# Performance work log

Measured on AMD Instinct MI355X. Metric: run time of the kernel, lower is better.

The kernel has to match this reference:

```python
import jax, jax.numpy as jnp
import numpy as np

Z_DIM = 3
H = 128
N_BLOCKS = 4
N = 30000
E = 180000
T = 2


def _mlp2(x, W1, b1, W2, b2):
    return jnp.maximum(x @ W1 + b1, 0.0) @ W2 + b2


def _stats(x, eps=1e-8):
    # batch mean/std as accumulated by the running-stat Normalizer (buffers -> no grad)
    m = x.mean(0)
    v = jnp.maximum((x * x).mean(0) - m * m, 0.0)
    s = jnp.maximum(jnp.sqrt(v), eps)
    return jax.lax.stop_gradient(m), jax.lax.stop_gradient(s)


def setup_inputs() -> dict:
    key = jax.random.key(0)
    ks = jax.random.split(key, 32)

    def w(k, shape, fan_in):
        return jax.random.normal(k, shape, jnp.float32) / np.sqrt(fan_in).astype(np.float32)

    inp = {}
    inp["z"] = jax.random.normal(ks[0], (T, N, Z_DIM), jnp.float32)
    inp["z_target"] = jax.random.normal(ks[1], (N, Z_DIM), jnp.float32)
    inp["pos"] = jax.random.uniform(ks[2], (N, 2), jnp.float32)
    # encoder node MLP: z_dim -> H -> H
    inp["enc_node_W1"] = w(ks[3], (Z_DIM, H), Z_DIM)
    inp["enc_node_b1"] = jnp.zeros((H,), jnp.float32)
    inp["enc_node_W2"] = w(ks[4], (H, H), H)
    inp["enc_node_b2"] = jnp.zeros((H,), jnp.float32)
    # encoder edge MLP: edge_dim(3) -> H -> H
    inp["enc_edge_W1"] = w(ks[5], (3, H), 3)
    inp["enc_edge_b1"] = jnp.zeros((H,), jnp.float32)
    inp["enc_edge_W2"] = w(ks[6], (H, H), H)
    inp["enc_edge_b2"] = jnp.zeros((H,), jnp.float32)
    # decoder MLP: H -> H -> z_dim
    inp["dec_W1"] = w(ks[7], (H, H), H)
    inp["dec_b1"] = jnp.zeros((H,), jnp.float32)
    inp["dec_W2"] = w(ks[8], (H, Z_DIM), H)
    inp["dec_b2"] = jnp.zeros((Z_DIM,), jnp.float32)
    # GraphNetBlocks, stacked over n_blocks
    inp["blk_edge_W1"] = w(ks[9], (N_BLOCKS, 3 * H, H), 3 * H)
    inp["blk_edge_b1"] = jnp.zeros((N_BLOCKS, H), jnp.float32)
    inp["blk_edge_W2"] = w(ks[10], (N_BLOCKS, H, H), H)
    inp["blk_edge_b2"] = jnp.zeros((N_BLOCKS, H), jnp.float32)
    inp["blk_node_W1"] = w(ks[11], (N_BLOCKS, 2 * H, H), 2 * H)
    inp["blk_node_b1"] = jnp.zeros((N_BLOCKS, H), jnp.float32)
    inp["blk_node_W2"] = w(ks[12], (N_BLOCKS, H, H), H)
    inp["blk_node_b2"] = jnp.zeros((N_BLOCKS, H), jnp.float32)
    # bidirectional mesh edges (triangles_to_edges output)
    inp["senders"] = jax.random.randint(ks[13], (E,), 0, N, jnp.int64)
    inp["receivers"] = jax.random.randint(ks[14], (E,), 0, N, jnp.int64)
    return inp


def reference(z, z_target, pos,
              enc_node_W1, enc_node_b1, enc_node_W2, enc_node_b2,
              enc_edge_W1, enc_edge_b1, enc_edge_W2, enc_edge_b2,
              dec_W1, dec_b1, dec_W2, dec_b2,
              blk_edge_W1, blk_edge_b1, blk_edge_W2, blk_edge_b2,
              blk_node_W1, blk_node_b1, blk_node_W2, blk_node_b2,
              senders, receivers):
    zl = z[-1]                                   # [N, z_dim]
    n_nodes = zl.shape[0]

    # --- build_graph ---
    rel = pos[senders] - pos[receivers]          # [E, 2]
    ef_raw = jnp.concatenate([rel, jnp.linalg.norm(rel, axis=1, keepdims=True)], axis=1)  # [E, 3]
    em, es = _stats(ef_raw)
    ef = _mlp2((ef_raw - em) / es, enc_edge_W1, enc_edge_b1, enc_edge_W2, enc_edge_b2)    # [E, H]
    nm, ns = _stats(zl)
    nf = _mlp2((zl - nm) / ns, enc_node_W1, enc_node_b1, enc_node_W2, enc_node_b2)        # [N, H]

    # --- message passing blocks ---
    def block(carry, p):
        nf, ef = carry
        eW1, eb1, eW2, eb2, nW1, nb1, nW2, nb2 = p
        e_in = jnp.concatenate([ef, nf[senders], nf[receivers]], axis=1)   # [E, 3H]
        ef = _mlp2(e_in, eW1, eb1, eW2, eb2) + ef
        agg = jax.ops.segment_sum(ef, receivers, num_segments=n_nodes)    # [N, H]
        n_in = jnp.concatenate([nf, agg], axis=1)                          # [N, 2H]
        nf = _mlp2(n_in, nW1, nb1, nW2, nb2) + nf
        return (nf, ef), None

    (nf, ef), _ = jax.lax.scan(block, (nf, ef),
                               (blk_edge_W1, blk_edge_b1, blk_edge_W2, blk_edge_b2,
                                blk_node_W1, blk_node_b1, blk_node_W2, blk_node_b2))

    # --- decode + loss ---
    output = _mlp2(nf, dec_W1, dec_b1, dec_W2, dec_b2)                     # [N, z_dim]
    target = z_target - zl
    om, os = _stats(target)
    target_normalized = (target - om) / os
    loss = jnp.mean((target_normalized - output) ** 2)

    z_update = jax.lax.stop_gradient(output) * os + om                     # Normalizer.inverse(detach)
    z_pred = zl + z_update
    rmse = jnp.mean(jnp.sqrt(jnp.mean((z_pred - z_target) ** 2, axis=0)))
    return z_pred, loss, rmse
```

## Files before the change

### kernel.cpp

```cpp
#include <hip/hip_runtime.h>
#include <hip/hip_bf16.h>
#include <math.h>

#define HDIM 128
#define TPB 256

typedef __attribute__((ext_vector_type(8))) short bf16x8;
typedef __attribute__((ext_vector_type(4))) float f32x4;

static inline int ceil_div(int a, int b){ return (a + b - 1) / b; }

__device__ __forceinline__ float wave_sum(float v){
#pragma unroll
  for (int o = 32; o > 0; o >>= 1) v += __shfl_down(v, o, 64);
  return v;
}

__device__ __forceinline__ short f2bf(float f){
  __hip_bfloat16 h = __float2bfloat16(f);
  return *reinterpret_cast<short*>(&h);
}
__device__ __forceinline__ float bfb2f(short s){
  unsigned int u = ((unsigned int)(unsigned short)s) << 16;
  return __builtin_bit_cast(float, u);
}

__device__ __forceinline__ void gl_lds16(const short* g, short* l){
  __builtin_amdgcn_global_load_lds(
      (const __attribute__((address_space(1))) void*)g,
      (__attribute__((address_space(3))) void*)l, 16, 0, 0);
}

__global__ void csr_hist(const int* __restrict__ rcv, int* __restrict__ deg, int E){
  int e = blockIdx.x * blockDim.x + threadIdx.x;
  if (e < E) atomicAdd(&deg[rcv[e]], 1);
}

__global__ void csr_scan(const int* __restrict__ deg, int* __restrict__ row_start,
                         int N, int E){
  __shared__ int part[1024];
  int t = threadIdx.x;
  int chunk = (N + 1023) / 1024;
  int lo = t * chunk, hi = min(lo + chunk, N);
  int s = 0;
  for (int i = lo; i < hi; i++) s += deg[i];
  part[t] = s;
  __syncthreads();
  for (int off = 1; off < 1024; off <<= 1){
    int v = (t >= off) ? part[t - off] : 0;
    __syncthreads();
    part[t] += v;
    __syncthreads();
  }
  int base = (t == 0) ? 0 : part[t - 1];
  for (int i = lo; i < hi; i++){
    row_start[i] = base;
    base += deg[i];
  }
  if (t == 1023) row_start[N] = E;
}

__global__ void csr_scatter(const int* __restrict__ snd,
                            const int* __restrict__ rcv,
                            int* __restrict__ cursor,
                            int* __restrict__ pinv,
                            int* __restrict__ psnd,
                            int* __restrict__ prcv, int E){
  int e = blockIdx.x * blockDim.x + threadIdx.x;
  if (e < E){
    int r = rcv[e];
    int p = atomicAdd(&cursor[r], 1);
    pinv[e] = p;
    psnd[p] = snd[e];
    prcv[p] = r;
  }
}

__global__ void edge_raw_stats(const float* __restrict__ pos,
                               const int* __restrict__ snd,
                               const int* __restrict__ rcv,
                               const int* __restrict__ pinv,
                               float* __restrict__ ef_raw,
                               float* __restrict__ epart, int E){
  __shared__ float red[4][6];
  int tid = threadIdx.x, w = tid >> 6, l = tid & 63;
  int e = blockIdx.x * blockDim.x + tid;
  float s[6] = {0.f,0.f,0.f,0.f,0.f,0.f};
  if (e < E){
    int si = snd[e], ri = rcv[e];
    float rx = pos[2*si]   - pos[2*ri];
    float ry = pos[2*si+1] - pos[2*ri+1];
    float nm = sqrtf(rx*rx + ry*ry);
    int p = pinv[e];
    ef_raw[3*p]   = rx;
    ef_raw[3*p+1] = ry;
    ef_raw[3*p+2] = nm;
    s[0] = rx; s[1] = ry; s[2] = nm;
    s[3] = rx*rx; s[4] = ry*ry; s[5] = nm*nm;
  }
#pragma unroll
  for (int k = 0; k < 6; k++) s[k] = wave_sum(s[k]);
  if (l == 0)
#pragma unroll
    for (int k = 0; k < 6; k++) red[w][k] = s[k];
  __syncthreads();
  if (tid < 6)
    epart[(size_t)blockIdx.x * 6 + tid] =
      red[0][tid] + red[1][tid] + red[2][tid] + red[3][tid];
}

__global__ void node_stats(const float* __restrict__ zl,
                           const float* __restrict__ z_target,
                           float* __restrict__ npart, int N){
  __shared__ float red[4][12];
  int tid = threadIdx.x, w = tid >> 6, l = tid & 63;
  int n = blockIdx.x * blockDim.x + tid;
  float s[12];
#pragma unroll
  for (int i = 0; i < 12; i++) s[i] = 0.f;
  if (n < N){
#pragma unroll
    for (int d = 0; d < 3; d++){
      float z = zl[3*n+d];
      float t = z_target[3*n+d] - z;
      s[d]   = z;  s[3+d] = z*z;
      s[6+d] = t;  s[9+d] = t*t;
    }
  }
#pragma unroll
  for (int i = 0; i < 12; i++) s[i] = wave_sum(s[i]);
  if (l == 0)
#pragma unroll
    for (int i = 0; i < 12; i++) red[w][i] = s[i];
  __syncthreads();
  if (tid < 12)
    npart[(size_t)blockIdx.x * 12 + tid] =
      red[0][tid] + red[1][tid] + red[2][tid] + red[3][tid];
}

__global__ void reduce_stats(const float* __restrict__ ep, int ne,
                             const float* __restrict__ np_, int nn,
                             float* __restrict__ raw){
  __shared__ float red[4];
  int tid = threadIdx.x, w = tid >> 6, l = tid & 63;
  for (int j = 0; j < 6; j++){
    float s = 0.f;
    for (int b = tid; b < ne; b += 256) s += ep[(size_t)b * 6 + j];
    s = wave_sum(s);
    if (l == 0) red[w] = s;
    __syncthreads();
    if (tid == 0) raw[j] = red[0] + red[1] + red[2] + red[3];
    __syncthreads();
  }
  for (int j = 0; j < 12; j++){
    float s = 0.f;
    for (int b = tid; b < nn; b += 256) s += np_[(size_t)b * 12 + j];
    s = wave_sum(s);
    if (l == 0) red[w] = s;
    __syncthreads();
    if (tid == 0) raw[6 + j] = red[0] + red[1] + red[2] + red[3];
    __syncthreads();
  }
}

__global__ void finalize_stats(const float* __restrict__ raw,
                               float* __restrict__ fin, int E, int N){
#pragma unroll
  for (int d = 0; d < 3; d++){
    float cE = (float)E, cN = (float)N;
    float m, v;
    m = raw[0+d] / cE; v = fmaxf(raw[3+d]/cE - m*m, 0.f);
    fin[0+d] = m;  fin[3+d]  = fmaxf(sqrtf(v), 1e-8f);
    m = raw[6+d] / cN; v = fmaxf(raw[9+d]/cN - m*m, 0.f);
    fin[6+d] = m;  fin[9+d]  = fmaxf(sqrtf(v), 1e-8f);
    m = raw[12+d] / cN; v = fmaxf(raw[15+d]/cN - m*m, 0.f);
    fin[12+d] = m; fin[15+d] = fmaxf(sqrtf(v), 1e-8f);
  }
}

__global__ void pack_weights(const float* __restrict__ encEW2,
                             const float* __restrict__ encNW2,
                             const float* __restrict__ decW1,
                             const float* __restrict__ beW1,
                             const float* __restrict__ beW2,
                             const float* __restrict__ bnW1,
                             const float* __restrict__ bnW2,
                             __hip_bfloat16* __restrict__ wp){
  int y = blockIdx.y;
  const float* src; __hip_bfloat16* dst; int K;
  if (y == 0){ src = encEW2; dst = wp;          K = 128; }
  else if (y == 1){ src = encNW2; dst = wp + 16384; K = 128; }
  else if (y == 2){ src = decW1;  dst = wp + 32768; K = 128; }
  else {
    int b = (y - 3) >> 2, j = (y - 3) & 3;
    __hip_bfloat16* base = wp + 49152 + b * 114688;
    if (j == 0){ src = beW1 + b*49152; dst = base;          K = 384; }
    else if (j == 1){ src = beW2 + b*16384; dst = base + 49152; K = 128; }
    else if (j == 2){ src = bnW1 + b*32768; dst = base + 65536; K = 256; }
    else { src = bnW2 + b*16384; dst = base + 98304; K = 128; }
  }
  int id = blockIdx.x * blockDim.x + threadIdx.x;
  if (id >= 128 * K) return;
  int c = id >> 12;
  int r = id & 4095;
  int t = r >> 9;
  int l = (r >> 3) & 63;
  int j = r & 7;
  int k = c * 32 + ((l >> 4) << 3) + j;
  int n = t * 16 + (l & 15);
  dst[id] = __float2bfloat16(src[k * 128 + n]);
}

__launch_bounds__(256)
__global__ void encoder_fused(const float* __restrict__ raw,
                              const float* __restrict__ mptr,
                              const float* __restrict__ sptr,
                              const float* __restrict__ W1,
                              const float* __restrict__ b1,
                              const __hip_bfloat16* __restrict__ W2f,
                              const float* __restrict__ b2,
                              __hip_bfloat16* __restrict__ out, int rows){
  __shared__ __align__(16) short bsh[16384];
  const int tid = threadIdx.x, w = tid >> 6, l = tid & 63, m = l & 15, q = l >> 4;
  const short* wsrc = (const short*)W2f;
#pragma unroll
  for (int i = 0; i < 8; i++){
    int inst = w * 8 + i;
    gl_lds16(wsrc + inst * 512 + l * 8, &bsh[inst * 512]);
  }
  float s0 = mptr[0], s1 = mptr[1], s2 = mptr[2];
  float d0 = sptr[0], d1 = sptr[1], d2 = sptr[2];
  const int row0 = blockIdx.x * 64 + w * 16;
  const int ra = min(row0 + m, rows - 1);
  float x0 = (raw[3*ra]   - s0) / d0;
  float x1 = (raw[3*ra+1] - s1) / d1;
  float x2 = (raw[3*ra+2] - s2) / d2;
  bf16x8 afr[4];
#pragma unroll
  for (int c = 0; c < 4; c++){
    int nb = c * 32 + q * 8;
#pragma unroll
    for (int j = 0; j < 8; j++){
      float h = b1[nb+j] + x0 * W1[nb+j] + x1 * W1[128+nb+j] + x2 * W1[256+nb+j];
      afr[c][j] = f2bf(fmaxf(h, 0.f));
    }
  }
  f32x4 acc[8];
#pragma unroll
  for (int t = 0; t < 8; t++) acc[t] = (f32x4){0.f,0.f,0.f,0.f};
  __syncthreads();
#pragma unroll
  for (int c = 0; c < 4; c++){
#pragma unroll
    for (int t = 0; t < 8; t++){
      bf16x8 b = *(const bf16x8*)&bsh[(c*8 + t)*512 + l*8];
      acc[t] = __builtin_amdgcn_mfma_f32_16x16x32_bf16(afr[c], b, acc[t], 0, 0, 0);
    }
  }
  const int row_d = row0 + q * 4;
#pragma unroll
  for (int t = 0; t < 8; t++){
    int col = t * 16 + m;
    float bb = b2[col];
#pragma unroll
    for (int r = 0; r < 4; r++){
      int e = row_d + r;
      if (e < rows) out[(size_t)e * HDIM + col] = __float2bfloat16(acc[t][r] + bb);
    }
  }
}

__launch_bounds__(256)
__global__ void gemm128_g(const __hip_bfloat16* __restrict__ A,
                          const __hip_bfloat16* __restrict__ Wf,
                          const float* __restrict__ bias,
                          float* __restrict__ out, int rows){
  __shared__ __align__(16) short bsh[16384];
  const int tid = threadIdx.x, w = tid >> 6, l = tid & 63, m = l & 15, q = l >> 4;
  const short* wsrc = (const short*)Wf;
#pragma unroll
  for (int i = 0; i < 8; i++){
    int inst = w * 8 + i;
    gl_lds16(wsrc + inst * 512 + l * 8, &bsh[inst * 512]);
  }
  const int row0 = blockIdx.x * 64 + w * 16;
  const int ra = min(row0 + m, rows - 1);
  const short* pa = (const short*)A + (size_t)ra * HDIM + q * 8;
  bf16x8 afr[4];
#pragma unroll
  for (int c = 0; c < 4; c++) afr[c] = *(const bf16x8*)(pa + c * 32);
  f32x4 acc[8];
#pragma unroll
  for (int t = 0; t < 8; t++) acc[t] = (f32x4){0.f,0.f,0.f,0.f};
  __syncthreads();
#pragma unroll
  for (int c = 0; c < 4; c++){
#pragma unroll
    for (int t = 0; t < 8; t++){
      bf16x8 b = *(const bf16x8*)&bsh[(c*8 + t)*512 + l*8];
      acc[t] = __builtin_amdgcn_mfma_f32_16x16x32_bf16(afr[c], b, acc[t], 0, 0, 0);
    }
  }
  const int row_d = row0 + q * 4;
#pragma unroll
  for (int t = 0; t < 8; t++){
    int col = t * 16 + m;
    float bb = bias[col];
#pragma unroll
    for (int r = 0; r < 4; r++){
      int e = row_d + r;
      if (e < rows) out[(size_t)e * HDIM + col] = fmaxf(acc[t][r] + bb, 0.f);
    }
  }
}

__launch_bounds__(512)
__global__ void edge_block(const int* __restrict__ psnd,
                           const int* __restrict__ prcv,
                           const __hip_bfloat16* __restrict__ nf,
                           __hip_bfloat16* __restrict__ ef,
                           const __hip_bfloat16* __restrict__ Wfrag,
                           const float* __restrict__ b1,
                           const float* __restrict__ b2,
                           int E){
  __shared__ __align__(16) short bsh[2][4096];
  __shared__ __align__(16) short hsh[8][16][136];
  const int tid = threadIdx.x, w = tid >> 6, l = tid & 63, m = l & 15, q = l >> 4;
  const short* wsrc = (const short*)Wfrag;
  gl_lds16(wsrc + w*512 + l*8, &bsh[0][w*512]);

  const int row0 = blockIdx.x * 128 + w * 16;
  const int ra = min(row0 + m, E - 1);
  const int si = psnd[ra], ri = prcv[ra];
  const short* pe = (const short*)ef + (size_t)ra * HDIM + q * 8;
  const short* ps = (const short*)nf + (size_t)si * HDIM + q * 8;
  const short* pr = (const short*)nf + (size_t)ri * HDIM + q * 8;
  bf16x8 afr[12];
#pragma unroll
  for (int c = 0; c < 4; c++){
    afr[c]   = *(const bf16x8*)(pe + c * 32);
    afr[4+c] = *(const bf16x8*)(ps + c * 32);
    afr[8+c] = *(const bf16x8*)(pr + c * 32);
  }
  f32x4 acc[8];
#pragma unroll
  for (int t = 0; t < 8; t++) acc[t] = (f32x4){0.f,0.f,0.f,0.f};
  __syncthreads();
#pragma unroll
  for (int c = 0; c < 12; c++){
    gl_lds16(wsrc + (c+1)*4096 + w*512 + l*8, &bsh[(c+1)&1][w*512]);
    const short* bb = &bsh[c & 1][0];
#pragma unroll
    for (int t = 0; t < 8; t++){
      bf16x8 b = *(const bf16x8*)(bb + t*512 + l*8);
      acc[t] = __builtin_amdgcn_mfma_f32_16x16x32_bf16(afr[c], b, acc[t], 0, 0, 0);
    }
    __syncthreads();
  }
#pragma unroll
  for (int t = 0; t < 8; t++){
    float bb = b1[t * 16 + m];
#pragma unroll
    for (int r = 0; r < 4; r++)
      hsh[w][q*4 + r][t*16 + m] = f2bf(fmaxf(acc[t][r] + bb, 0.f));
  }
  const short* ph = &hsh[w][m][0] + q * 8;
  f32x4 acc2[8];
#pragma unroll
  for (int t = 0; t < 8; t++) acc2[t] = (f32x4){0.f,0.f,0.f,0.f};
#pragma unroll
  for (int c = 12; c < 16; c++){
    if (c + 1 < 16)
      gl_lds16(wsrc + (c+1)*4096 + w*512 + l*8, &bsh[(c+1)&1][w*512]);
    bf16x8 a = *(const bf16x8*)(ph + (c - 12) * 32);
    const short* bb = &bsh[c & 1][0];
#pragma unroll
    for (int t = 0; t < 8; t++){
      bf16x8 b = *(const bf16x8*)(bb + t*512 + l*8);
      acc2[t] = __builtin_amdgcn_mfma_f32_16x16x32_bf16(a, b, acc2[t], 0, 0, 0);
    }
    if (c < 15) __syncthreads();
  }
#pragma unroll
  for (int t = 0; t < 8; t++){
    float bb = b2[t * 16 + m];
#pragma unroll
    for (int r = 0; r < 4; r++)
      hsh[w][q*4 + r][t*16 + m] = f2bf(acc2[t][r] + bb);
  }
  int orow = row0 + (l >> 2);
  if (orow < E){
    const short* src = &hsh[w][l >> 2][(l & 3) * 32];
    short* dst = (short*)ef + (size_t)orow * HDIM + (l & 3) * 32;
#pragma unroll
    for (int k = 0; k < 4; k++){
      bf16x8 vnew = *(const bf16x8*)(src + k * 8);
      bf16x8 vold = *(const bf16x8*)(dst + k * 8);
      bf16x8 vo;
#pragma unroll
      for (int j = 0; j < 8; j++) vo[j] = f2bf(bfb2f(vnew[j]) + bfb2f(vold[j]));
      *(bf16x8*)(dst + k * 8) = vo;
    }
  }
}

__launch_bounds__(512)
__global__ void node_block(const int* __restrict__ row_start,
                           const __hip_bfloat16* __restrict__ ef,
                           __hip_bfloat16* __restrict__ nf,
                           const __hip_bfloat16* __restrict__ Wfrag,
                           const float* __restrict__ b1,
                           const float* __restrict__ b2,
                           int N){
  __shared__ __align__(16) short bsh[2][4096];
  __shared__ __align__(16) short hsh[8][16][136];
  const int tid = threadIdx.x, w = tid >> 6, l = tid & 63, m = l & 15, q = l >> 4;
  const short* wsrc = (const short*)Wfrag;
  gl_lds16(wsrc + w*512 + l*8, &bsh[0][w*512]);

  const int row0 = blockIdx.x * 128 + w * 16;
  const int ra = min(row0 + m, N - 1);
  const short* pn = (const short*)nf + (size_t)ra * HDIM + q * 8;
  bf16x8 afr[8];
#pragma unroll
  for (int c = 0; c < 4; c++) afr[c] = *(const bf16x8*)(pn + c * 32);
  float sum[4][8];
#pragma unroll
  for (int c = 0; c < 4; c++)
#pragma unroll
    for (int j = 0; j < 8; j++) sum[c][j] = 0.f;
  int s0 = row_start[ra], s1 = row_start[ra + 1];
  for (int it = s0; it < s1; it++){
    const short* pf = (const short*)ef + (size_t)it * HDIM + q * 8;
#pragma unroll
    for (int c = 0; c < 4; c++){
      bf16x8 v = *(const bf16x8*)(pf + c * 32);
#pragma unroll
      for (int j = 0; j < 8; j++) sum[c][j] += bfb2f(v[j]);
    }
  }
#pragma unroll
  for (int c = 0; c < 4; c++)
#pragma unroll
    for (int j = 0; j < 8; j++) afr[4 + c][j] = f2bf(sum[c][j]);

  f32x4 acc[8];
#pragma unroll
  for (int t = 0; t < 8; t++) acc[t] = (f32x4){0.f,0.f,0.f,0.f};
  __syncthreads();
#pragma unroll
  for (int c = 0; c < 8; c++){
    gl_lds16(wsrc + (c+1)*4096 + w*512 + l*8, &bsh[(c+1)&1][w*512]);
    const short* bb = &bsh[c & 1][0];
#pragma unroll
    for (int t = 0; t < 8; t++){
      bf16x8 b = *(const bf16x8*)(bb + t*512 + l*8);
      acc[t] = __builtin_amdgcn_mfma_f32_16x16x32_bf16(afr[c], b, acc[t], 0, 0, 0);
    }
    __syncthreads();
  }
#pragma unroll
  for (int t = 0; t < 8; t++){
    float bb = b1[t * 16 + m];
#pragma unroll
    for (int r = 0; r < 4; r++)
      hsh[w][q*4 + r][t*16 + m] = f2bf(fmaxf(acc[t][r] + bb, 0.f));
  }
  const short* ph = &hsh[w][m][0] + q * 8;
  f32x4 acc2[8];
#pragma unroll
  for (int t = 0; t < 8; t++) acc2[t] = (f32x4){0.f,0.f,0.f,0.f};
#pragma unroll
  for (int c = 8; c < 12; c++){
    if (c + 1 < 12)
      gl_lds16(wsrc + (c+1)*4096 + w*512 + l*8, &bsh[(c+1)&1][w*512]);
    bf16x8 a = *(const bf16x8*)(ph + (c - 8) * 32);
    const short* bb = &bsh[c & 1][0];
#pragma unroll
    for (int t = 0; t < 8; t++){
      bf16x8 b = *(const bf16x8*)(bb + t*512 + l*8);
      acc2[t] = __builtin_amdgcn_mfma_f32_16x16x32_bf16(a, b, acc2[t], 0, 0, 0);
    }
    if (c < 11) __syncthreads();
  }
#pragma unroll
  for (int t = 0; t < 8; t++){
    float bb = b2[t * 16 + m];
#pragma unroll
    for (int r = 0; r < 4; r++)
      hsh[w][q*4 + r][t*16 + m] = f2bf(acc2[t][r] + bb);
  }
  int orow = row0 + (l >> 2);
  if (orow < N){
    const short* src = &hsh[w][l >> 2][(l & 3) * 32];
    short* dst = (short*)nf + (size_t)orow * HDIM + (l & 3) * 32;
#pragma unroll
    for (int k = 0; k < 4; k++){
      bf16x8 vnew = *(const bf16x8*)(src + k * 8);
      bf16x8 vold = *(const bf16x8*)(dst + k * 8);
      bf16x8 vo;
#pragma unroll
      for (int j = 0; j < 8; j++) vo[j] = f2bf(bfb2f(vnew[j]) + bfb2f(vold[j]));
      *(bf16x8*)(dst + k * 8) = vo;
    }
  }
}

__global__ void dec_final(const float* __restrict__ hbuf,
                          const float* __restrict__ W2,
                          const float* __restrict__ b2,
                          float* __restrict__ outd, int rows){
  __shared__ float hl[64 * 129];
  __shared__ float Wl[HDIM * 3];
  __shared__ float bl[3];
  int t = threadIdx.x;
  int node0 = blockIdx.x * 64;
  for (int i = t; i < HDIM * 3; i += 256) Wl[i] = W2[i];
  if (t < 3) bl[t] = b2[t];
#pragma unroll
  for (int i = 0; i < 32; i++){
    int lin = t + i * 256;
    int r = lin >> 7;
    int c = lin & 127;
    int node = node0 + r;
    hl[r * 129 + c] = (node < rows) ? hbuf[(size_t)node * HDIM + c] : 0.f;
  }
  __syncthreads();
  if (t < 64){
    int node = node0 + t;
    if (node < rows){
      float a0 = bl[0], a1 = bl[1], a2 = bl[2];
      for (int k = 0; k < HDIM; k++){
        float v = hl[t * 129 + k];
        a0 += v * Wl[k * 3];
        a1 += v * Wl[k * 3 + 1];
        a2 += v * Wl[k * 3 + 2];
      }
      outd[3 * node]     = a0;
      outd[3 * node + 1] = a1;
      outd[3 * node + 2] = a2;
    }
  }
}

__global__ void epilogue(const float* __restrict__ dec_out,
                         const float* __restrict__ zl,
                         const float* __restrict__ z_target,
                         const float* __restrict__ fin,
                         float* __restrict__ d_out,
                         float* __restrict__ lpart, int N){
  __shared__ float red[4][4];
  int tid = threadIdx.x, w = tid >> 6, l = tid & 63;
  int n = blockIdx.x * blockDim.x + tid;
  float s[4] = {0.f,0.f,0.f,0.f};
  if (n < N){
#pragma unroll
    for (int d = 0; d < 3; d++){
      float om = fin[12 + d], os = fin[15 + d];
      float o   = dec_out[3*n + d];
      float zld = zl[3*n + d];
      float zt  = z_target[3*n + d];
      float tgt = zt - zld;
      float tn  = (tgt - om) / os;
      float diff = tn - o;
      s[0] += diff * diff;
      float zp = zld + o * os + om;
      d_out[3*n + d] = zp;
      float e = zp - zt;
      s[1 + d] = e * e;
    }
  }
#pragma unroll
  for (int k = 0; k < 4; k++) s[k] = wave_sum(s[k]);
  if (l == 0)
#pragma unroll
    for (int k = 0; k < 4; k++) red[w][k] = s[k];
  __syncthreads();
  if (tid < 4)
    lpart[(size_t)blockIdx.x * 4 + tid] =
      red[0][tid] + red[1][tid] + red[2][tid] + red[3][tid];
}

__global__ void finalize_out(const float* __restrict__ lpart, int nb,
                             float* __restrict__ d_out, int N){
  __shared__ float red[4];
  __shared__ float vals[4];
  int tid = threadIdx.x, w = tid >> 6, l = tid & 63;
  for (int j = 0; j < 4; j++){
    float s = 0.f;
    for (int b = tid; b < nb; b += 256) s += lpart[(size_t)b * 4 + j];
    s = wave_sum(s);
    if (l == 0) red[w] = s;
    __syncthreads();
    if (tid == 0) vals[j] = red[0] + red[1] + red[2] + red[3];
    __syncthreads();
  }
  if (tid == 0){
    float cN = (float)N;
    float loss = vals[0] / (3.f * cN);
    float rmse = (sqrtf(vals[1] / cN) + sqrtf(vals[2] / cN) + sqrtf(vals[3] / cN)) / 3.f;
    d_out[(size_t)3 * N]     = loss;
    d_out[(size_t)3 * N + 1] = rmse;
  }
}

extern "C" void kernel_launch(void* const* d_in, const int* in_sizes, int n_in,
                              void* d_out, int out_size, void* d_ws, size_t ws_size,
                              hipStream_t stream){
  const float* z           = (const float*)d_in[0];
  const float* z_target    = (const float*)d_in[1];
  const float* pos         = (const float*)d_in[2];
  const float* enc_node_W1 = (const float*)d_in[3];
  const float* enc_node_b1 = (const float*)d_in[4];
  const float* enc_node_W2 = (const float*)d_in[5];
  const float* enc_node_b2 = (const float*)d_in[6];
  const float* enc_edge_W1 = (const float*)d_in[7];
  const float* enc_edge_b1 = (const float*)d_in[8];
  const float* enc_edge_W2 = (const float*)d_in[9];
  const float* enc_edge_b2 = (const float*)d_in[10];
  const float* dec_W1      = (const float*)d_in[11];
  const float* dec_b1      = (const float*)d_in[12];
  const float* dec_W2      = (const float*)d_in[13];
  const float* dec_b2      = (const float*)d_in[14];
  const float* blk_edge_W1 = (const float*)d_in[15];
  const float* blk_edge_b1 = (const float*)d_in[16];
  const float* blk_edge_W2 = (const float*)d_in[17];
  const float* blk_edge_b2 = (const float*)d_in[18];
  const float* blk_node_W1 = (const float*)d_in[19];
  const float* blk_node_b1 = (const float*)d_in[20];
  const float* blk_node_W2 = (const float*)d_in[21];
  const float* blk_node_b2 = (const float*)d_in[22];
  const int*   senders     = (const int*)d_in[23];
  const int*   receivers   = (const int*)d_in[24];

  const int N = in_sizes[1] / 3;
  const int E = in_sizes[23];
  const float* zl = z + (size_t)N * 3;

  const int neb = ceil_div(E, TPB);
  const int nnb = ceil_div(N, TPB);

  char* p = (char*)d_ws;
  auto carve = [&](size_t bytes) -> char* {
    char* r = p; p += (bytes + 255) & ~(size_t)255; return r;
  };
  float* stats_raw = (float*)carve(32 * 4);
  float* stats_fin = (float*)carve(32 * 4);
  float* epart     = (float*)carve((size_t)neb * 6 * 4);
  float* npart     = (float*)carve((size_t)nnb * 12 * 4);
  float* lpart     = (float*)carve((size_t)nnb * 4 * 4);
  float* ef_raw    = (float*)carve((size_t)E * 3 * 4);
  float* dec_out   = (float*)carve((size_t)N * 3 * 4);
  float* hbuf      = (float*)carve((size_t)N * HDIM * 4);
  int*   deg       = (int*)carve((size_t)N * 4);
  int*   row_start = (int*)carve((size_t)(N + 1) * 4);
  int*   cursor    = (int*)carve((size_t)N * 4);
  int*   pinv      = (int*)carve((size_t)E * 4);
  int*   psnd      = (int*)carve((size_t)E * 4);
  int*   prcv      = (int*)carve((size_t)E * 4);
  __hip_bfloat16* wp = (__hip_bfloat16*)carve((size_t)507904 * 2);
  __hip_bfloat16* ef = (__hip_bfloat16*)carve((size_t)E * HDIM * 2);
  __hip_bfloat16* nf = (__hip_bfloat16*)carve((size_t)N * HDIM * 2);

  float* out = (float*)d_out;

  hipMemsetAsync(deg, 0, (size_t)N * 4, stream);

  csr_hist<<<neb, TPB, 0, stream>>>(receivers, deg, E);
  csr_scan<<<1, 1024, 0, stream>>>(deg, row_start, N, E);
  hipMemcpyAsync(cursor, row_start, (size_t)N * 4, hipMemcpyDeviceToDevice, stream);
  csr_scatter<<<neb, TPB, 0, stream>>>(senders, receivers, cursor, pinv, psnd, prcv, E);

  edge_raw_stats<<<neb, TPB, 0, stream>>>(pos, senders, receivers, pinv, ef_raw, epart, E);
  node_stats<<<nnb, TPB, 0, stream>>>(zl, z_target, npart, N);
  reduce_stats<<<1, TPB, 0, stream>>>(epart, neb, npart, nnb, stats_raw);
  finalize_stats<<<1, 1, 0, stream>>>(stats_raw, stats_fin, E, N);

  pack_weights<<<dim3(192, 19), TPB, 0, stream>>>(enc_edge_W2, enc_node_W2, dec_W1,
                                                  blk_edge_W1, blk_edge_W2,
                                                  blk_node_W1, blk_node_W2, wp);

  encoder_fused<<<ceil_div(E, 64), TPB, 0, stream>>>(ef_raw, stats_fin + 0, stats_fin + 3,
                                                     enc_edge_W1, enc_edge_b1,
                                                     wp, enc_edge_b2, ef, E);
  encoder_fused<<<ceil_div(N, 64), TPB, 0, stream>>>(zl, stats_fin + 6, stats_fin + 9,
                                                     enc_node_W1, enc_node_b1,
                                                     wp + 16384, enc_node_b2, nf, N);

  for (int b = 0; b < 4; b++){
    const __hip_bfloat16* eWf = wp + 49152 + (size_t)b * 114688;
    const __hip_bfloat16* nWf = eWf + 65536;
    const float* eb1 = blk_edge_b1 + (size_t)b * 128;
    const float* eb2 = blk_edge_b2 + (size_t)b * 128;
    const float* nb1 = blk_node_b1 + (size_t)b * 128;
    const float* nb2 = blk_node_b2 + (size_t)b * 128;

    edge_block<<<ceil_div(E, 128), 512, 0, stream>>>(psnd, prcv, nf, ef,
                                                     eWf, eb1, eb2, E);
    node_block<<<ceil_div(N, 128), 512, 0, stream>>>(row_start, ef, nf,
                                                     nWf, nb1, nb2, N);
  }

  gemm128_g<<<ceil_div(N, 64), TPB, 0, stream>>>(nf, wp + 32768, dec_b1, hbuf, N);
  dec_final<<<ceil_div(N, 64), TPB, 0, stream>>>(hbuf, dec_W2, dec_b2, dec_out, N);

  epilogue<<<nnb, TPB, 0, stream>>>(dec_out, zl, z_target, stats_fin,
                                    out, lpart, N);
  finalize_out<<<1, TPB, 0, stream>>>(lpart, nnb, out, N);
}
```

Before: 573.8 us.

## Process two row tiles per wave, read weight fragments from global, fuse CSR scatter

Edge and node block kernels now use 256-thread blocks in which each wave handles two 16-row tiles. Weight fragments are loaded directly from global memory (L1/L2-cached) and each one feeds two MFMAs, so the LDS double-buffered weight staging and its per-chunk __syncthreads are gone. The CSR scatter is fused into the edge raw-stats kernel, which removes one launch and the pinv array. The cost is higher register pressure from two accumulator sets and weight reads that now depend on the cache instead of LDS.

```diff
diff --git a/kernel.cpp b/kernel.cpp
--- a/kernel.cpp
+++ b/kernel.cpp
@@ -60,38 +60,26 @@
   if (t == 1023) row_start[N] = E;
 }
 
-__global__ void csr_scatter(const int* __restrict__ snd,
-                            const int* __restrict__ rcv,
-                            int* __restrict__ cursor,
-                            int* __restrict__ pinv,
-                            int* __restrict__ psnd,
-                            int* __restrict__ prcv, int E){
-  int e = blockIdx.x * blockDim.x + threadIdx.x;
-  if (e < E){
-    int r = rcv[e];
-    int p = atomicAdd(&cursor[r], 1);
-    pinv[e] = p;
-    psnd[p] = snd[e];
-    prcv[p] = r;
-  }
-}
-
-__global__ void edge_raw_stats(const float* __restrict__ pos,
-                               const int* __restrict__ snd,
-                               const int* __restrict__ rcv,
-                               const int* __restrict__ pinv,
-                               float* __restrict__ ef_raw,
-                               float* __restrict__ epart, int E){
+__global__ void edge_prep(const float* __restrict__ pos,
+                          const int* __restrict__ snd,
+                          const int* __restrict__ rcv,
+                          int* __restrict__ cursor,
+                          int* __restrict__ psnd,
+                          int* __restrict__ prcv,
+                          float* __restrict__ ef_raw,
+                          float* __restrict__ epart, int E){
   __shared__ float red[4][6];
   int tid = threadIdx.x, w = tid >> 6, l = tid & 63;
   int e = blockIdx.x * blockDim.x + tid;
   float s[6] = {0.f,0.f,0.f,0.f,0.f,0.f};
   if (e < E){
     int si = snd[e], ri = rcv[e];
+    int p = atomicAdd(&cursor[ri], 1);
+    psnd[p] = si;
+    prcv[p] = ri;
     float rx = pos[2*si]   - pos[2*ri];
     float ry = pos[2*si+1] - pos[2*ri+1];
     float nm = sqrtf(rx*rx + ry*ry);
-    int p = pinv[e];
     ef_raw[3*p]   = rx;
     ef_raw[3*p+1] = ry;
     ef_raw[3*p+2] = nm;
@@ -314,7 +302,7 @@
   }
 }
 
-__launch_bounds__(512)
+__launch_bounds__(256, 4)
 __global__ void edge_block(const int* __restrict__ psnd,
                            const int* __restrict__ prcv,
                            const __hip_bfloat16* __restrict__ nf,
@@ -323,88 +311,91 @@
                            const float* __restrict__ b1,
                            const float* __restrict__ b2,
                            int E){
-  __shared__ __align__(16) short bsh[2][4096];
-  __shared__ __align__(16) short hsh[8][16][136];
+  __shared__ __align__(16) short hsh[4][2][16][136];
   const int tid = threadIdx.x, w = tid >> 6, l = tid & 63, m = l & 15, q = l >> 4;
-  const short* wsrc = (const short*)Wfrag;
-  gl_lds16(wsrc + w*512 + l*8, &bsh[0][w*512]);
-
-  const int row0 = blockIdx.x * 128 + w * 16;
-  const int ra = min(row0 + m, E - 1);
-  const int si = psnd[ra], ri = prcv[ra];
-  const short* pe = (const short*)ef + (size_t)ra * HDIM + q * 8;
-  const short* ps = (const short*)nf + (size_t)si * HDIM + q * 8;
-  const short* pr = (const short*)nf + (size_t)ri * HDIM + q * 8;
-  bf16x8 afr[12];
-#pragma unroll
-  for (int c = 0; c < 4; c++){
-    afr[c]   = *(const bf16x8*)(pe + c * 32);
-    afr[4+c] = *(const bf16x8*)(ps + c * 32);
-    afr[8+c] = *(const bf16x8*)(pr + c * 32);
-  }
-  f32x4 acc[8];
-#pragma unroll
-  for (int t = 0; t < 8; t++) acc[t] = (f32x4){0.f,0.f,0.f,0.f};
-  __syncthreads();
+  const short* wb = (const short*)Wfrag;
+  const int row0 = blockIdx.x * 128 + w * 32;
+  const int ra0 = min(row0 + m, E - 1);
+  const int ra1 = min(row0 + 16 + m, E - 1);
+  const int s0i = psnd[ra0], r0i = prcv[ra0];
+  const int s1i = psnd[ra1], r1i = prcv[ra1];
+  const short* pe0 = (const short*)ef + (size_t)ra0 * HDIM + q * 8;
+  const short* pe1 = (const short*)ef + (size_t)ra1 * HDIM + q * 8;
+  const short* ps0 = (const short*)nf + (size_t)s0i * HDIM + q * 8;
+  const short* ps1 = (const short*)nf + (size_t)s1i * HDIM + q * 8;
+  const short* pr0 = (const short*)nf + (size_t)r0i * HDIM + q * 8;
+  const short* pr1 = (const short*)nf + (size_t)r1i * HDIM + q * 8;
+
+  f32x4 acc0[8], acc1[8];
+#pragma unroll
+  for (int t = 0; t < 8; t++){ acc0[t] = (f32x4){0,0,0,0}; acc1[t] = (f32x4){0,0,0,0}; }
 #pragma unroll
   for (int c = 0; c < 12; c++){
-    gl_lds16(wsrc + (c+1)*4096 + w*512 + l*8, &bsh[(c+1)&1][w*512]);
-    const short* bb = &bsh[c & 1][0];
+    const short* pa0 = (c < 4 ? pe0 : (c < 8 ? ps0 : pr0)) + (c & 3) * 32;
+    const short* pa1 = (c < 4 ? pe1 : (c < 8 ? ps1 : pr1)) + (c & 3) * 32;
+    bf16x8 a0 = *(const bf16x8*)pa0;
+    bf16x8 a1 = *(const bf16x8*)pa1;
 #pragma unroll
     for (int t = 0; t < 8; t++){
-      bf16x8 b = *(const bf16x8*)(bb + t*512 + l*8);
-      acc[t] = __builtin_amdgcn_mfma_f32_16x16x32_bf16(afr[c], b, acc[t], 0, 0, 0);
-    }
-    __syncthreads();
+      bf16x8 b = *(const bf16x8*)(wb + ((c*8 + t)*64 + l)*8);
+      acc0[t] = __builtin_amdgcn_mfma_f32_16x16x32_bf16(a0, b, acc0[t], 0, 0, 0);
+      acc1[t] = __builtin_amdgcn_mfma_f32_16x16x32_bf16(a1, b, acc1[t], 0, 0, 0);
+    }
   }
 #pragma unroll
   for (int t = 0; t < 8; t++){
     float bb = b1[t * 16 + m];
 #pragma unroll
-    for (int r = 0; r < 4; r++)
-      hsh[w][q*4 + r][t*16 + m] = f2bf(fmaxf(acc[t][r] + bb, 0.f));
-  }
-  const short* ph = &hsh[w][m][0] + q * 8;
-  f32x4 acc2[8];
-#pragma unroll
-  for (int t = 0; t < 8; t++) acc2[t] = (f32x4){0.f,0.f,0.f,0.f};
-#pragma unroll
-  for (int c = 12; c < 16; c++){
-    if (c + 1 < 16)
-      gl_lds16(wsrc + (c+1)*4096 + w*512 + l*8, &bsh[(c+1)&1][w*512]);
-    bf16x8 a = *(const bf16x8*)(ph + (c - 12) * 32);
-    const short* bb = &bsh[c & 1][0];
+    for (int r = 0; r < 4; r++){
+      hsh[w][0][q*4 + r][t*16 + m] = f2bf(fmaxf(acc0[t][r] + bb, 0.f));
+      hsh[w][1][q*4 + r][t*16 + m] = f2bf(fmaxf(acc1[t][r] + bb, 0.f));
+    }
+  }
+  const short* ph0 = &hsh[w][0][m][0] + q * 8;
+  const short* ph1 = &hsh[w][1][m][0] + q * 8;
+  f32x4 acc2a[8], acc2b[8];
+#pragma unroll
+  for (int t = 0; t < 8; t++){ acc2a[t] = (f32x4){0,0,0,0}; acc2b[t] = (f32x4){0,0,0,0}; }
+#pragma unroll
+  for (int c = 0; c < 4; c++){
+    bf16x8 a0 = *(const bf16x8*)(ph0 + c * 32);
+    bf16x8 a1 = *(const bf16x8*)(ph1 + c * 32);
 #pragma unroll
     for (int t = 0; t < 8; t++){
-      bf16x8 b = *(const bf16x8*)(bb + t*512 + l*8);
-      acc2[t] = __builtin_amdgcn_mfma_f32_16x16x32_bf16(a, b, acc2[t], 0, 0, 0);
-    }
-    if (c < 15) __syncthreads();
+      bf16x8 b = *(const bf16x8*)(wb + 49152 + ((c*8 + t)*64 + l)*8);
+      acc2a[t] = __builtin_amdgcn_mfma_f32_16x16x32_bf16(a0, b, acc2a[t], 0, 0, 0);
+      acc2b[t] = __builtin_amdgcn_mfma_f32_16x16x32_bf16(a1, b, acc2b[t], 0, 0, 0);
+    }
   }
 #pragma unroll
   for (int t = 0; t < 8; t++){
     float bb = b2[t * 16 + m];
 #pragma unroll
-    for (int r = 0; r < 4; r++)
-      hsh[w][q*4 + r][t*16 + m] = f2bf(acc2[t][r] + bb);
-  }
-  int orow = row0 + (l >> 2);
-  if (orow < E){
-    const short* src = &hsh[w][l >> 2][(l & 3) * 32];
-    short* dst = (short*)ef + (size_t)orow * HDIM + (l & 3) * 32;
-#pragma unroll
-    for (int k = 0; k < 4; k++){
-      bf16x8 vnew = *(const bf16x8*)(src + k * 8);
-      bf16x8 vold = *(const bf16x8*)(dst + k * 8);
-      bf16x8 vo;
-#pragma unroll
-      for (int j = 0; j < 8; j++) vo[j] = f2bf(bfb2f(vnew[j]) + bfb2f(vold[j]));
-      *(bf16x8*)(dst + k * 8) = vo;
-    }
-  }
-}
-
-__launch_bounds__(512)
+    for (int r = 0; r < 4; r++){
+      hsh[w][0][q*4 + r][t*16 + m] = f2bf(acc2a[t][r] + bb);
+      hsh[w][1][q*4 + r][t*16 + m] = f2bf(acc2b[t][r] + bb);
+    }
+  }
+#pragma unroll
+  for (int tile = 0; tile < 2; tile++){
+    int orow = row0 + tile * 16 + (l >> 2);
+    if (orow < E){
+      const short* src = &hsh[w][tile][l >> 2][(l & 3) * 32];
+      short* dst = (short*)ef + (size_t)orow * HDIM + (l & 3) * 32;
+#pragma unroll
+      for (int k = 0; k < 4; k++){
+        bf16x8 vnew = *(const bf16x8*)(src + k * 8);
+        bf16x8 vold = *(const bf16x8*)(dst + k * 8);
+        bf16x8 vo;
+#pragma unroll
+        for (int j = 0; j < 8; j++) vo[j] = f2bf(bfb2f(vnew[j]) + bfb2f(vold[j]));
+        *(bf16x8*)(dst + k * 8) = vo;
+      }
+    }
+  }
+}
+
+__launch_bounds__(256)
 __global__ void node_block(const int* __restrict__ row_start,
                            const __hip_bfloat16* __restrict__ ef,
                            __hip_bfloat16* __restrict__ nf,
@@ -412,96 +403,122 @@
                            const float* __restrict__ b1,
                            const float* __restrict__ b2,
                            int N){
-  __shared__ __align__(16) short bsh[2][4096];
-  __shared__ __align__(16) short hsh[8][16][136];
+  __shared__ __align__(16) short hsh[4][2][16][136];
   const int tid = threadIdx.x, w = tid >> 6, l = tid & 63, m = l & 15, q = l >> 4;
-  const short* wsrc = (const short*)Wfrag;
-  gl_lds16(wsrc + w*512 + l*8, &bsh[0][w*512]);
-
-  const int row0 = blockIdx.x * 128 + w * 16;
-  const int ra = min(row0 + m, N - 1);
-  const short* pn = (const short*)nf + (size_t)ra * HDIM + q * 8;
-  bf16x8 afr[8];
-#pragma unroll
-  for (int c = 0; c < 4; c++) afr[c] = *(const bf16x8*)(pn + c * 32);
-  float sum[4][8];
-#pragma unroll
-  for (int c = 0; c < 4; c++)
-#pragma unroll
-    for (int j = 0; j < 8; j++) sum[c][j] = 0.f;
-  int s0 = row_start[ra], s1 = row_start[ra + 1];
-  for (int it = s0; it < s1; it++){
-    const short* pf = (const short*)ef + (size_t)it * HDIM + q * 8;
-#pragma unroll
-    for (int c = 0; c < 4; c++){
-      bf16x8 v = *(const bf16x8*)(pf + c * 32);
-#pragma unroll
-      for (int j = 0; j < 8; j++) sum[c][j] += bfb2f(v[j]);
-    }
-  }
-#pragma unroll
-  for (int c = 0; c < 4; c++)
-#pragma unroll
-    for (int j = 0; j < 8; j++) afr[4 + c][j] = f2bf(sum[c][j]);
-
-  f32x4 acc[8];
-#pragma unroll
-  for (int t = 0; t < 8; t++) acc[t] = (f32x4){0.f,0.f,0.f,0.f};
-  __syncthreads();
+  const short* wb = (const short*)Wfrag;
+  const int row0 = blockIdx.x * 128 + w * 32;
+  const int ra0 = min(row0 + m, N - 1);
+  const int ra1 = min(row0 + 16 + m, N - 1);
+  const short* pn0 = (const short*)nf + (size_t)ra0 * HDIM + q * 8;
+  const short* pn1 = (const short*)nf + (size_t)ra1 * HDIM + q * 8;
+
+  bf16x8 ag0[4], ag1[4];
+  {
+    float sum[4][8];
+#pragma unroll
+    for (int c = 0; c < 4; c++)
+#pragma unroll
+      for (int j = 0; j < 8; j++) sum[c][j] = 0.f;
+    int s0 = row_start[ra0], s1 = row_start[ra0 + 1];
+    for (int it = s0; it < s1; it++){
+      const short* pf = (const short*)ef + (size_t)it * HDIM + q * 8;
+#pragma unroll
+      for (int c = 0; c < 4; c++){
+        bf16x8 v = *(const bf16x8*)(pf + c * 32);
+#pragma unroll
+        for (int j = 0; j < 8; j++) sum[c][j] += bfb2f(v[j]);
+      }
+    }
+#pragma unroll
+    for (int c = 0; c < 4; c++)
+#pragma unroll
+      for (int j = 0; j < 8; j++) ag0[c][j] = f2bf(sum[c][j]);
+  }
+  {
+    float sum[4][8];
+#pragma unroll
+    for (int c = 0; c < 4; c++)
+#pragma unroll
+      for (int j = 0; j < 8; j++) sum[c][j] = 0.f;
+    int s0 = row_start[ra1], s1 = row_start[ra1 + 1];
+    for (int it = s0; it < s1; it++){
+      const short* pf = (const short*)ef + (size_t)it * HDIM + q * 8;
+#pragma unroll
+      for (int c = 0; c < 4; c++){
+        bf16x8 v = *(const bf16x8*)(pf + c * 32);
+#pragma unroll
+        for (int j = 0; j < 8; j++) sum[c][j] += bfb2f(v[j]);
+      }
+    }
+#pragma unroll
+    for (int c = 0; c < 4; c++)
+#pragma unroll
+      for (int j = 0; j < 8; j++) ag1[c][j] = f2bf(sum[c][j]);
+  }
+
+  f32x4 acc0[8], acc1[8];
+#pragma unroll
+  for (int t = 0; t < 8; t++){ acc0[t] = (f32x4){0,0,0,0}; acc1[t] = (f32x4){0,0,0,0}; }
 #pragma unroll
   for (int c = 0; c < 8; c++){
-    gl_lds16(wsrc + (c+1)*4096 + w*512 + l*8, &bsh[(c+1)&1][w*512]);
-    const short* bb = &bsh[c & 1][0];
+    bf16x8 a0 = (c < 4) ? *(const bf16x8*)(pn0 + c * 32) : ag0[c - 4];
+    bf16x8 a1 = (c < 4) ? *(const bf16x8*)(pn1 + c * 32) : ag1[c - 4];
 #pragma unroll
     for (int t = 0; t < 8; t++){
-      bf16x8 b = *(const bf16x8*)(bb + t*512 + l*8);
-      acc[t] = __builtin_amdgcn_mfma_f32_16x16x32_bf16(afr[c], b, acc[t], 0, 0, 0);
-    }
-    __syncthreads();
+      bf16x8 b = *(const bf16x8*)(wb + ((c*8 + t)*64 + l)*8);
+      acc0[t] = __builtin_amdgcn_mfma_f32_16x16x32_bf16(a0, b, acc0[t], 0, 0, 0);
+      acc1[t] = __builtin_amdgcn_mfma_f32_16x16x32_bf16(a1, b, acc1[t], 0, 0, 0);
+    }
   }
 #pragma unroll
   for (int t = 0; t < 8; t++){
     float bb = b1[t * 16 + m];
 #pragma unroll
-    for (int r = 0; r < 4; r++)
-      hsh[w][q*4 + r][t*16 + m] = f2bf(fmaxf(acc[t][r] + bb, 0.f));
-  }
-  const short* ph = &hsh[w][m][0] + q * 8;
-  f32x4 acc2[8];
-#pragma unroll
-  for (int t = 0; t < 8; t++) acc2[t] = (f32x4){0.f,0.f,0.f,0.f};
-#pragma unroll
-  for (int c = 8; c < 12; c++){
-    if (c + 1 < 12)
-      gl_lds16(wsrc + (c+1)*4096 + w*512 + l*8, &bsh[(c+1)&1][w*512]);
-    bf16x8 a = *(const bf16x8*)(ph + (c - 8) * 32);
-    const short* bb = &bsh[c & 1][0];
+    for (int r = 0; r < 4; r++){
+      hsh[w][0][q*4 + r][t*16 + m] = f2bf(fmaxf(acc0[t][r] + bb, 0.f));
+      hsh[w][1][q*4 + r][t*16 + m] = f2bf(fmaxf(acc1[t][r] + bb, 0.f));
+    }
+  }
+  const short* ph0 = &hsh[w][0][m][0] + q * 8;
+  const short* ph1 = &hsh[w][1][m][0] + q * 8;
+  f32x4 acc2a[8], acc2b[8];
+#pragma unroll
+  for (int t = 0; t < 8; t++){ acc2a[t] = (f32x4){0,0,0,0}; acc2b[t] = (f32x4){0,0,0,0}; }
+#pragma unroll
+  for (int c = 0; c < 4; c++){
+    bf16x8 a0 = *(const bf16x8*)(ph0 + c * 32);
+    bf16x8 a1 = *(const bf16x8*)(ph1 + c * 32);
 #pragma unroll
     for (int t = 0; t < 8; t++){
-      bf16x8 b = *(const bf16x8*)(bb + t*512 + l*8);
-      acc2[t] = __builtin_amdgcn_mfma_f32_16x16x32_bf16(a, b, acc2[t], 0, 0, 0);
-    }
-    if (c < 11) __syncthreads();
+      bf16x8 b = *(const bf16x8*)(wb + 32768 + ((c*8 + t)*64 + l)*8);
+      acc2a[t] = __builtin_amdgcn_mfma_f32_16x16x32_bf16(a0, b, acc2a[t], 0, 0, 0);
+      acc2b[t] = __builtin_amdgcn_mfma_f32_16x16x32_bf16(a1, b, acc2b[t], 0, 0, 0);
+    }
   }
 #pragma unroll
   for (int t = 0; t < 8; t++){
     float bb = b2[t * 16 + m];
 #pragma unroll
-    for (int r = 0; r < 4; r++)
-      hsh[w][q*4 + r][t*16 + m] = f2bf(acc2[t][r] + bb);
-  }
-  int orow = row0 + (l >> 2);
-  if (orow < N){
-    const short* src = &hsh[w][l >> 2][(l & 3) * 32];
-    short* dst = (short*)nf + (size_t)orow * HDIM + (l & 3) * 32;
-#pragma unroll
-    for (int k = 0; k < 4; k++){
-      bf16x8 vnew = *(const bf16x8*)(src + k * 8);
-      bf16x8 vold = *(const bf16x8*)(dst + k * 8);
-      bf16x8 vo;
-#pragma unroll
-      for (int j = 0; j < 8; j++) vo[j] = f2bf(bfb2f(vnew[j]) + bfb2f(vold[j]));
-      *(bf16x8*)(dst + k * 8) = vo;
+    for (int r = 0; r < 4; r++){
+      hsh[w][0][q*4 + r][t*16 + m] = f2bf(acc2a[t][r] + bb);
+      hsh[w][1][q*4 + r][t*16 + m] = f2bf(acc2b[t][r] + bb);
+    }
+  }
+#pragma unroll
+  for (int tile = 0; tile < 2; tile++){
+    int orow = row0 + tile * 16 + (l >> 2);
+    if (orow < N){
+      const short* src = &hsh[w][tile][l >> 2][(l & 3) * 32];
+      short* dst = (short*)nf + (size_t)orow * HDIM + (l & 3) * 32;
+#pragma unroll
+      for (int k = 0; k < 4; k++){
+        bf16x8 vnew = *(const bf16x8*)(src + k * 8);
+        bf16x8 vold = *(const bf16x8*)(dst + k * 8);
+        bf16x8 vo;
+#pragma unroll
+        for (int j = 0; j < 8; j++) vo[j] = f2bf(bfb2f(vnew[j]) + bfb2f(vold[j]));
+        *(bf16x8*)(dst + k * 8) = vo;
+      }
     }
   }
 }
@@ -655,7 +672,6 @@
   int*   deg       = (int*)carve((size_t)N * 4);
   int*   row_start = (int*)carve((size_t)(N + 1) * 4);
   int*   cursor    = (int*)carve((size_t)N * 4);
-  int*   pinv      = (int*)carve((size_t)E * 4);
   int*   psnd      = (int*)carve((size_t)E * 4);
   int*   prcv      = (int*)carve((size_t)E * 4);
   __hip_bfloat16* wp = (__hip_bfloat16*)carve((size_t)507904 * 2);
@@ -669,9 +685,9 @@
   csr_hist<<<neb, TPB, 0, stream>>>(receivers, deg, E);
   csr_scan<<<1, 1024, 0, stream>>>(deg, row_start, N, E);
   hipMemcpyAsync(cursor, row_start, (size_t)N * 4, hipMemcpyDeviceToDevice, stream);
-  csr_scatter<<<neb, TPB, 0, stream>>>(senders, receivers, cursor, pinv, psnd, prcv, E);
-
-  edge_raw_stats<<<neb, TPB, 0, stream>>>(pos, senders, receivers, pinv, ef_raw, epart, E);
+  edge_prep<<<neb, TPB, 0, stream>>>(pos, senders, receivers, cursor,
+                                     psnd, prcv, ef_raw, epart, E);
+
   node_stats<<<nnb, TPB, 0, stream>>>(zl, z_target, npart, N);
   reduce_stats<<<1, TPB, 0, stream>>>(epart, neb, npart, nnb, stats_raw);
   finalize_stats<<<1, 1, 0, stream>>>(stats_raw, stats_fin, E, N);
@@ -695,9 +711,9 @@
     const float* nb1 = blk_node_b1 + (size_t)b * 128;
     const float* nb2 = blk_node_b2 + (size_t)b * 128;
 
-    edge_block<<<ceil_div(E, 128), 512, 0, stream>>>(psnd, prcv, nf, ef,
+    edge_block<<<ceil_div(E, 128), TPB, 0, stream>>>(psnd, prcv, nf, ef,
                                                      eWf, eb1, eb2, E);
-    node_block<<<ceil_div(N, 128), 512, 0, stream>>>(row_start, ef, nf,
+    node_block<<<ceil_div(N, 128), TPB, 0, stream>>>(row_start, ef, nf,
                                                      nWf, nb1, nb2, N);
   }
 
```

Measured after the change: 764.6 us. +33.3%, slower.
